# Kernel optimization log

Hardware: AMD Instinct MI355X
Metric: run time of the kernel (lower is better)

Reference implementation:

```python
import jax, jax.numpy as jnp
import numpy as np
from jax import lax

S = 2048      # num_states
V = 32768     # num_observations
T = 4096      # sequence length


def setup_inputs() -> dict:
    key = jax.random.key(0)
    k_obs, k_a, k_b, k_pi = jax.random.split(key, 4)
    observations = jax.random.randint(k_obs, (T,), 0, V)
    # A: row-stochastic so the unnormalized alpha recursion stays finite over T steps.
    A = jax.random.uniform(k_a, (S, S), dtype=jnp.float32)
    A = A / jnp.sum(A, axis=1, keepdims=True)
    # B: emission factors near 1 to avoid exponential under/overflow.
    B = jax.random.uniform(k_b, (S, V), dtype=jnp.float32, minval=0.9, maxval=1.1)
    pi = jax.random.uniform(k_pi, (S,), dtype=jnp.float32)
    return {"observations": observations, "A": A, "B": B, "pi": pi}


def reference(observations, A, B, pi):
    # Gather emission columns once: [T, S]
    B_obs = B[:, observations].T
    alpha0 = pi * B_obs[0]  # [S]

    def step(alpha, b_t):
        # alpha_t = (alpha_{t-1} @ A) * B[:, obs_t]
        alpha_new = jnp.matmul(alpha, A) * b_t
        return alpha_new, None

    alpha_T, _ = lax.scan(step, alpha0, B_obs[1:])
    return jnp.sum(alpha_T)
```

## Files before the change

kernel.cpp:

```cpp
#include <hip/hip_runtime.h>


#define S 2048
#define V 32768
#define T 4096
#define G 128
#define BT 512
#define COLS 16
#define RING 16
#define DIST 8

#define SM_AS    0
#define SM_AL    32768
#define SM_BR    (SM_AL + 2560)
#define SM_WP    (SM_BR + RING * COLS)
#define SM_FP    (SM_WP + 8 * COLS)
#define SMEM_FLOATS (SM_FP + 8)
#define SMEM_BYTES  (SMEM_FLOATS * 4)

__global__ __launch_bounds__(BT, 1) void hmm_fwd(
    const int* __restrict__ obs,
    const float* __restrict__ A,
    const float* __restrict__ B,
    const float* __restrict__ pi,
    float* __restrict__ out,
    unsigned long long* __restrict__ buf)
{
    extern __shared__ float smem[];
    float4* As4    = (float4*)(smem + SM_AS);
    float4* al4    = (float4*)(smem + SM_AL);
    float*  bring  = smem + SM_BR;
    float*  wpart  = smem + SM_WP;
    float*  fpart  = smem + SM_FP;

    const int g    = blockIdx.x;
    const int tid  = threadIdx.x;
    const int lane = tid & 63;
    const int wave = tid >> 6;
    const int cq   = tid & 3;
    const int rg   = tid >> 2;

    {
        const int u  = tid & 3;
        const int r0 = tid >> 2;
        for (int it = 0; it < 16; ++it) {
            int r = r0 + 128 * it;
            float4 av = *(const float4*)(A + (size_t)r * S + g * COLS + 4 * u);
            As4[(r * 4 + u) ^ ((r >> 4) & 7)] = av;
        }
    }

    if (wave == 1 && lane < COLS) {
        int jj = g * COLS + lane;
        for (int u = 1; u <= DIST; ++u) {
            int o = obs[u];
            bring[(u & (RING - 1)) * COLS + lane] = B[(size_t)jj * V + o];
        }
    }
    if (wave == 0 && lane < COLS) {
        int jl = g * COLS + lane;
        int o0 = obs[0];
        float v = pi[jl] * B[(size_t)jl * V + o0];
        unsigned long long p = (1ull << 32) | (unsigned long long)__float_as_uint(v);
        __hip_atomic_store(&buf[jl], p, __ATOMIC_RELAXED, __HIP_MEMORY_SCOPE_AGENT);
    }

    __syncthreads();

    for (int t = 1; t < T; ++t) {
        float4 af[16];
#pragma unroll
        for (int r = 0; r < 16; ++r)
            af[r] = As4[((rg * 16 + r) * 4 + cq) ^ (rg & 7)];
#pragma unroll
        for (int r = 0; r < 16; ++r)
            asm volatile("" : "+v"(af[r].x), "+v"(af[r].y),
                              "+v"(af[r].z), "+v"(af[r].w));

        unsigned long long want = (unsigned long long)t;
        unsigned long long* src = buf + (((t - 1) & 1) * S) + 4 * tid;
        unsigned long long v0, v1, v2, v3;
        for (;;) {
            v0 = __hip_atomic_load(&src[0], __ATOMIC_RELAXED, __HIP_MEMORY_SCOPE_AGENT);
            v1 = __hip_atomic_load(&src[1], __ATOMIC_RELAXED, __HIP_MEMORY_SCOPE_AGENT);
            v2 = __hip_atomic_load(&src[2], __ATOMIC_RELAXED, __HIP_MEMORY_SCOPE_AGENT);
            v3 = __hip_atomic_load(&src[3], __ATOMIC_RELAXED, __HIP_MEMORY_SCOPE_AGENT);
            if ((v0 >> 32) == want && (v1 >> 32) == want &&
                (v2 >> 32) == want && (v3 >> 32) == want) break;
            __builtin_amdgcn_s_sleep(1);
        }
        float4 f;
        f.x = __uint_as_float((unsigned)v0);
        f.y = __uint_as_float((unsigned)v1);
        f.z = __uint_as_float((unsigned)v2);
        f.w = __uint_as_float((unsigned)v3);
        al4[tid + (tid >> 2)] = f;
        __syncthreads();

        if (wave == 1 && lane < COLS) {
            int tp = t + DIST;
            if (tp < T) {
                int o = obs[tp];
                bring[(tp & (RING - 1)) * COLS + lane] =
                    B[(size_t)(g * COLS + lane) * V + o];
            }
        }

        float4 acc = {0.f, 0.f, 0.f, 0.f};
#pragma unroll
        for (int k = 0; k < 4; ++k) {
            int p = rg * 4 + k;
            float4 al = al4[p + (p >> 2)];
            float4 a0 = af[4 * k + 0];
            float4 a1 = af[4 * k + 1];
            float4 a2 = af[4 * k + 2];
            float4 a3 = af[4 * k + 3];
            acc.x = fmaf(al.x, a0.x, acc.x);
            acc.x = fmaf(al.y, a1.x, acc.x);
            acc.x = fmaf(al.z, a2.x, acc.x);
            acc.x = fmaf(al.w, a3.x, acc.x);
            acc.y = fmaf(al.x, a0.y, acc.y);
            acc.y = fmaf(al.y, a1.y, acc.y);
            acc.y = fmaf(al.z, a2.y, acc.y);
            acc.y = fmaf(al.w, a3.y, acc.y);
            acc.z = fmaf(al.x, a0.z, acc.z);
            acc.z = fmaf(al.y, a1.z, acc.z);
            acc.z = fmaf(al.z, a2.z, acc.z);
            acc.z = fmaf(al.w, a3.z, acc.z);
            acc.w = fmaf(al.x, a0.w, acc.w);
            acc.w = fmaf(al.y, a1.w, acc.w);
            acc.w = fmaf(al.z, a2.w, acc.w);
            acc.w = fmaf(al.w, a3.w, acc.w);
        }
#pragma unroll
        for (int off = 32; off >= 4; off >>= 1) {
            acc.x += __shfl_down(acc.x, off, 64);
            acc.y += __shfl_down(acc.y, off, 64);
            acc.z += __shfl_down(acc.z, off, 64);
            acc.w += __shfl_down(acc.w, off, 64);
        }
        if (lane < 4)
            *(float4*)(wpart + wave * 16 + lane * 4) = acc;
        __syncthreads();

        if (wave == 0 && lane < 16) {
            float s = 0.f;
#pragma unroll
            for (int w = 0; w < 8; ++w) s += wpart[w * 16 + lane];
            float val = s * bring[(t & (RING - 1)) * COLS + lane];
            unsigned long long p = (((unsigned long long)(t + 1)) << 32) |
                                   (unsigned long long)__float_as_uint(val);
            __hip_atomic_store(&buf[(t & 1) * S + g * COLS + lane], p,
                               __ATOMIC_RELAXED, __HIP_MEMORY_SCOPE_AGENT);
        }
    }

    if (g == 0) {
        unsigned long long want = (unsigned long long)T;
        unsigned long long* src = buf + (((T - 1) & 1) * S) + 4 * tid;
        unsigned long long v0, v1, v2, v3;
        for (;;) {
            v0 = __hip_atomic_load(&src[0], __ATOMIC_RELAXED, __HIP_MEMORY_SCOPE_AGENT);
            v1 = __hip_atomic_load(&src[1], __ATOMIC_RELAXED, __HIP_MEMORY_SCOPE_AGENT);
            v2 = __hip_atomic_load(&src[2], __ATOMIC_RELAXED, __HIP_MEMORY_SCOPE_AGENT);
            v3 = __hip_atomic_load(&src[3], __ATOMIC_RELAXED, __HIP_MEMORY_SCOPE_AGENT);
            if ((v0 >> 32) == want && (v1 >> 32) == want &&
                (v2 >> 32) == want && (v3 >> 32) == want) break;
            __builtin_amdgcn_s_sleep(1);
        }
        float sm = __uint_as_float((unsigned)v0) + __uint_as_float((unsigned)v1) +
                   __uint_as_float((unsigned)v2) + __uint_as_float((unsigned)v3);
        sm += __shfl_down(sm, 32, 64);
        sm += __shfl_down(sm, 16, 64);
        sm += __shfl_down(sm, 8, 64);
        sm += __shfl_down(sm, 4, 64);
        sm += __shfl_down(sm, 2, 64);
        sm += __shfl_down(sm, 1, 64);
        if (lane == 0) fpart[wave] = sm;
        __syncthreads();
        if (tid == 0) {
            float tot = 0.f;
            for (int w = 0; w < 8; ++w) tot += fpart[w];
            out[0] = tot;
        }
    }
}

extern "C" void kernel_launch(void* const* d_in, const int* in_sizes, int n_in,
                              void* d_out, int out_size, void* d_ws, size_t ws_size,
                              hipStream_t stream) {
    const int*   obs = (const int*)d_in[0];
    const float* A   = (const float*)d_in[1];
    const float* B   = (const float*)d_in[2];
    const float* pi  = (const float*)d_in[3];
    float* out = (float*)d_out;
    unsigned long long* buf = (unsigned long long*)d_ws;

    hipFuncSetAttribute((const void*)hmm_fwd,
                        hipFuncAttributeMaxDynamicSharedMemorySize, SMEM_BYTES);


    void* args[] = { (void*)&obs, (void*)&A, (void*)&B, (void*)&pi,
                     (void*)&out, (void*)&buf };
    hipLaunchCooperativeKernel((void*)hmm_fwd, dim3(G), dim3(BT), args,
                               SMEM_BYTES, stream);
}
```

Before: 9.296 ms.

## Remove per-step block barrier by exchanging alpha within wavefront groups

Each thread now polls the global handoff buffer for exactly the alpha entries its 4-thread group needs, rather than a block-wide slice. The values are shared through LDS inside the wavefront, so the block-wide `__syncthreads` after staging alpha is no longer needed. The partial-sum scratch is double-buffered across steps so the one remaining barrier per step protects it. The A-tile swizzle is changed to keep LDS reads conflict-free under the new access pattern. The aim is to cut barrier latency on the serial recurrence's critical path, at the cost of relying on intra-wave LDS ordering.

```diff
diff --git a/kernel.cpp b/kernel.cpp
--- a/kernel.cpp
+++ b/kernel.cpp
@@ -11,12 +11,17 @@
 #define DIST 8
 
 #define SM_AS    0
-#define SM_AL    32768
-#define SM_BR    (SM_AL + 2560)
+#define SM_SH    32768
+#define SM_BR    (SM_SH + 2048)
 #define SM_WP    (SM_BR + RING * COLS)
-#define SM_FP    (SM_WP + 8 * COLS)
+#define SM_FP    (SM_WP + 2 * 128)
 #define SMEM_FLOATS (SM_FP + 8)
 #define SMEM_BYTES  (SMEM_FLOATS * 4)
+
+__device__ __forceinline__ int aswz(int row) {
+    int q = (row >> 4) & 7;
+    return ((q & 1) << 2) | (q >> 1);
+}
 
 __global__ __launch_bounds__(BT, 1) void hmm_fwd(
     const int* __restrict__ obs,
@@ -28,7 +33,7 @@
 {
     extern __shared__ float smem[];
     float4* As4    = (float4*)(smem + SM_AS);
-    float4* al4    = (float4*)(smem + SM_AL);
+    float4* sh4    = (float4*)(smem + SM_SH);
     float*  bring  = smem + SM_BR;
     float*  wpart  = smem + SM_WP;
     float*  fpart  = smem + SM_FP;
@@ -39,6 +44,7 @@
     const int wave = tid >> 6;
     const int cq   = tid & 3;
     const int rg   = tid >> 2;
+    const int sw   = ((rg & 1) << 2) | ((rg & 7) >> 1);
 
     {
         const int u  = tid & 3;
@@ -46,7 +52,7 @@
         for (int it = 0; it < 16; ++it) {
             int r = r0 + 128 * it;
             float4 av = *(const float4*)(A + (size_t)r * S + g * COLS + 4 * u);
-            As4[(r * 4 + u) ^ ((r >> 4) & 7)] = av;
+            As4[(r * 4 + u) ^ aswz(r)] = av;
         }
     }
 
@@ -71,14 +77,14 @@
         float4 af[16];
 #pragma unroll
         for (int r = 0; r < 16; ++r)
-            af[r] = As4[((rg * 16 + r) * 4 + cq) ^ (rg & 7)];
+            af[r] = As4[((rg * 16 + r) * 4 + cq) ^ sw];
 #pragma unroll
         for (int r = 0; r < 16; ++r)
             asm volatile("" : "+v"(af[r].x), "+v"(af[r].y),
                               "+v"(af[r].z), "+v"(af[r].w));
 
         unsigned long long want = (unsigned long long)t;
-        unsigned long long* src = buf + (((t - 1) & 1) * S) + 4 * tid;
+        unsigned long long* src = buf + (((t - 1) & 1) * S) + rg * 16 + cq * 4;
         unsigned long long v0, v1, v2, v3;
         for (;;) {
             v0 = __hip_atomic_load(&src[0], __ATOMIC_RELAXED, __HIP_MEMORY_SCOPE_AGENT);
@@ -94,8 +100,6 @@
         f.y = __uint_as_float((unsigned)v1);
         f.z = __uint_as_float((unsigned)v2);
         f.w = __uint_as_float((unsigned)v3);
-        al4[tid + (tid >> 2)] = f;
-        __syncthreads();
 
         if (wave == 1 && lane < COLS) {
             int tp = t + DIST;
@@ -106,32 +110,43 @@
             }
         }
 
+        sh4[tid] = f;
+        int qb = tid & ~3;
+        float4 al0 = sh4[qb + 0];
+        float4 al1 = sh4[qb + 1];
+        float4 al2 = sh4[qb + 2];
+        float4 al3 = sh4[qb + 3];
+
         float4 acc = {0.f, 0.f, 0.f, 0.f};
-#pragma unroll
-        for (int k = 0; k < 4; ++k) {
-            int p = rg * 4 + k;
-            float4 al = al4[p + (p >> 2)];
-            float4 a0 = af[4 * k + 0];
-            float4 a1 = af[4 * k + 1];
-            float4 a2 = af[4 * k + 2];
-            float4 a3 = af[4 * k + 3];
-            acc.x = fmaf(al.x, a0.x, acc.x);
-            acc.x = fmaf(al.y, a1.x, acc.x);
-            acc.x = fmaf(al.z, a2.x, acc.x);
-            acc.x = fmaf(al.w, a3.x, acc.x);
-            acc.y = fmaf(al.x, a0.y, acc.y);
-            acc.y = fmaf(al.y, a1.y, acc.y);
-            acc.y = fmaf(al.z, a2.y, acc.y);
-            acc.y = fmaf(al.w, a3.y, acc.y);
-            acc.z = fmaf(al.x, a0.z, acc.z);
-            acc.z = fmaf(al.y, a1.z, acc.z);
-            acc.z = fmaf(al.z, a2.z, acc.z);
-            acc.z = fmaf(al.w, a3.z, acc.z);
-            acc.w = fmaf(al.x, a0.w, acc.w);
-            acc.w = fmaf(al.y, a1.w, acc.w);
-            acc.w = fmaf(al.z, a2.w, acc.w);
-            acc.w = fmaf(al.w, a3.w, acc.w);
-        }
+#define DOT4(AL, B0)                                         \
+        {                                                    \
+            float4 a0 = af[(B0) + 0];                        \
+            float4 a1 = af[(B0) + 1];                        \
+            float4 a2 = af[(B0) + 2];                        \
+            float4 a3 = af[(B0) + 3];                        \
+            acc.x = fmaf(AL.x, a0.x, acc.x);                 \
+            acc.x = fmaf(AL.y, a1.x, acc.x);                 \
+            acc.x = fmaf(AL.z, a2.x, acc.x);                 \
+            acc.x = fmaf(AL.w, a3.x, acc.x);                 \
+            acc.y = fmaf(AL.x, a0.y, acc.y);                 \
+            acc.y = fmaf(AL.y, a1.y, acc.y);                 \
+            acc.y = fmaf(AL.z, a2.y, acc.y);                 \
+            acc.y = fmaf(AL.w, a3.y, acc.y);                 \
+            acc.z = fmaf(AL.x, a0.z, acc.z);                 \
+            acc.z = fmaf(AL.y, a1.z, acc.z);                 \
+            acc.z = fmaf(AL.z, a2.z, acc.z);                 \
+            acc.z = fmaf(AL.w, a3.z, acc.z);                 \
+            acc.w = fmaf(AL.x, a0.w, acc.w);                 \
+            acc.w = fmaf(AL.y, a1.w, acc.w);                 \
+            acc.w = fmaf(AL.z, a2.w, acc.w);                 \
+            acc.w = fmaf(AL.w, a3.w, acc.w);                 \
+        }
+        DOT4(al0, 0)
+        DOT4(al1, 4)
+        DOT4(al2, 8)
+        DOT4(al3, 12)
+#undef DOT4
+
 #pragma unroll
         for (int off = 32; off >= 4; off >>= 1) {
             acc.x += __shfl_down(acc.x, off, 64);
@@ -139,14 +154,15 @@
             acc.z += __shfl_down(acc.z, off, 64);
             acc.w += __shfl_down(acc.w, off, 64);
         }
+        float* wp = wpart + (t & 1) * 128;
         if (lane < 4)
-            *(float4*)(wpart + wave * 16 + lane * 4) = acc;
+            *(float4*)(wp + wave * 16 + lane * 4) = acc;
         __syncthreads();
 
         if (wave == 0 && lane < 16) {
             float s = 0.f;
 #pragma unroll
-            for (int w = 0; w < 8; ++w) s += wpart[w * 16 + lane];
+            for (int w = 0; w < 8; ++w) s += wp[w * 16 + lane];
             float val = s * bring[(t & (RING - 1)) * COLS + lane];
             unsigned long long p = (((unsigned long long)(t + 1)) << 32) |
                                    (unsigned long long)__float_as_uint(val);
```

Result: no change. 9.450 ms (+1.7%).
